# Performance work log

Hardware: AMD Instinct MI355X
Metric: run time of the kernel (lower is better)

The kernel has to match this reference:

```python
import jax, jax.numpy as jnp
import numpy as np

B, T, DIM, HEADS, MLP_H, R = 64, 197, 768, 12, 3072, 16
HD = DIM // HEADS
EPS = 1e-5
R_EFF = min(R, (T - 1) // 2)  # class token protected


def layernorm(x, g, b):
    m = jnp.mean(x, -1, keepdims=True)
    v = jnp.var(x, -1, keepdims=True)
    return (x - m) * jax.lax.rsqrt(v + EPS) * g + b


def matching_indices(metric):
    # metric: [B, T, HD]; class token (index 0 of 'a' set) protected
    metric = metric / jnp.linalg.norm(metric, axis=-1, keepdims=True)
    a, b = metric[:, ::2], metric[:, 1::2]            # [B,ta,d], [B,tb,d]
    scores = jnp.einsum('bic,bjc->bij', a, b)
    scores = scores.at[:, 0, :].set(-jnp.inf)         # protect cls token
    node_max = jnp.max(scores, axis=-1)
    node_idx = jnp.argmax(scores, axis=-1)
    edge_idx = jnp.argsort(-node_max, axis=-1)        # descending similarity
    unm_idx = edge_idx[:, R_EFF:]
    src_idx = edge_idx[:, :R_EFF]
    dst_idx = jnp.take_along_axis(node_idx, src_idx, axis=-1)
    unm_idx = jnp.sort(unm_idx, axis=1)               # keep cls first (cls token)
    return unm_idx, src_idx, dst_idx


def merge(x, unm_idx, src_idx, dst_idx):
    # x: [B, T, c] -> [B, T - R_EFF, c]; always scatter-add (as in source code)
    src, dst = x[:, ::2], x[:, 1::2]
    unm = jnp.take_along_axis(src, unm_idx[..., None], axis=1)
    sel = jnp.take_along_axis(src, src_idx[..., None], axis=1)
    bidx = jnp.arange(x.shape[0])[:, None]
    dst = dst.at[bidx, dst_idx].add(sel)
    return jnp.concatenate([unm, dst], axis=1)


def block(x, attn_size, ln1_g, ln1_b, w_qkv, w_proj, b_proj,
          ln2_g, ln2_b, w_fc1, b_fc1, w_fc2, b_fc2):
    # --- attention with log-size bias ---
    h = layernorm(x, ln1_g, ln1_b)
    qkv = (h @ w_qkv.T).reshape(B, T, 3, HEADS, HD).transpose(2, 0, 3, 1, 4)
    q, k, v = qkv[0], qkv[1], qkv[2]                  # [B,H,T,HD]
    attn = jnp.einsum('bhid,bhjd->bhij', q, k) * (HD ** -0.5)
    attn = attn + jnp.log(attn_size)[:, None, None, :, 0]
    attn = jax.nn.softmax(attn, axis=-1)
    o = jnp.einsum('bhij,bhjd->bhid', attn, v).transpose(0, 2, 1, 3).reshape(B, T, DIM)
    x = x + (o @ w_proj.T + b_proj)
    metric = jax.lax.stop_gradient(jnp.mean(k, axis=1))  # [B,T,HD]; no_grad in torch
    # --- ToMe bipartite soft matching ---
    unm_idx, src_idx, dst_idx = matching_indices(metric)
    # source tracking (adjacency initial tokens -> merged groups)
    source = jnp.broadcast_to(jnp.eye(T, dtype=x.dtype), (B, T, T))
    source = merge(source, unm_idx, src_idx, dst_idx)     # [B, Tn, T]
    tn = source.shape[1]
    rci = jnp.max(source * jnp.arange(1, tn + 1, dtype=x.dtype)[:, None], axis=-2)
    rci = (rci - 2.0)[:, 1:]                              # cls_token branch
    # size-weighted average merge
    xs = merge(x * attn_size, unm_idx, src_idx, dst_idx)
    new_size = merge(attn_size, unm_idx, src_idx, dst_idx)
    x = xs / new_size
    # --- MLP ---
    h2 = layernorm(x, ln2_g, ln2_b)
    h2 = jax.nn.gelu(h2 @ w_fc1.T + b_fc1, approximate=False)
    x = x + (h2 @ w_fc2.T + b_fc2)
    return x, new_size, rci


def setup_inputs() -> dict:
    key = jax.random.key(0)
    ks = jax.random.split(key, 6)
    return dict(
        x=jax.random.normal(ks[0], (B, T, DIM), jnp.float32),
        attn_size=jnp.ones((B, T, 1), jnp.float32),
        ln1_g=jnp.ones((DIM,), jnp.float32),
        ln1_b=jnp.zeros((DIM,), jnp.float32),
        w_qkv=jax.random.normal(ks[1], (3 * DIM, DIM), jnp.float32) * 0.02,
        w_proj=jax.random.normal(ks[2], (DIM, DIM), jnp.float32) * 0.02,
        b_proj=jnp.zeros((DIM,), jnp.float32),
        ln2_g=jnp.ones((DIM,), jnp.float32),
        ln2_b=jnp.zeros((DIM,), jnp.float32),
        w_fc1=jax.random.normal(ks[3], (MLP_H, DIM), jnp.float32) * 0.02,
        b_fc1=jnp.zeros((MLP_H,), jnp.float32),
        w_fc2=jax.random.normal(ks[4], (DIM, MLP_H), jnp.float32) * 0.02,
        b_fc2=jnp.zeros((DIM,), jnp.float32),
    )


def reference(x, attn_size, ln1_g, ln1_b, w_qkv, w_proj, b_proj,
              ln2_g, ln2_b, w_fc1, b_fc1, w_fc2, b_fc2):
    return block(x, attn_size, ln1_g, ln1_b, w_qkv, w_proj, b_proj,
                 ln2_g, ln2_b, w_fc1, b_fc1, w_fc2, b_fc2)
```

## Files before the change

kernel.cpp:

```cpp
#include <hip/hip_runtime.h>
#include <cstdint>
#include <cstddef>

#define DEVFN __device__ __forceinline__

typedef __attribute__((ext_vector_type(8))) short short8;
typedef __attribute__((ext_vector_type(4))) float f32x4;

#define GLOAD_LDS16(gaddr, laddr)                                              \
  __builtin_amdgcn_global_load_lds(                                            \
      (const __attribute__((address_space(1))) uint32_t*)(gaddr),              \
      (__attribute__((address_space(3))) uint32_t*)(laddr), 16, 0, 0)

constexpr int B_ = 64, T_ = 197, DIM_ = 768, H_ = 12, HD_ = 64, MLP_ = 3072;
constexpr int N_ = B_ * T_;
constexpr int NE_ = 99, NO_ = 98, REFF_ = 16;
constexpr int TM_ = (NE_ - REFF_) + NO_;
constexpr int NM_ = B_ * TM_;

constexpr size_t BOFF_A    = 0;
constexpr size_t BOFF_GBC  = 0;
constexpr size_t BOFF_B    = 58097664;
constexpr size_t BOFF_C    = 77463552;
constexpr size_t BOFF_D    = 113049600;
constexpr size_t BOFF_WKM  = 130842624;
constexpr size_t BOFF_RT   = 131039232;
constexpr size_t BOFF_NSZ  = 131873280;
constexpr size_t BOFF_WQB  = 131919616;
constexpr size_t BOFF_WPB  = 135458560;
constexpr size_t BOFF_W1B  = 136638208;
constexpr size_t BOFF_W2B  = 141356800;

DEVFN ushort f2b(float f) {
  union { float f; uint u; } c; c.f = f;
  uint u = c.u;
  u = (u + 0x7FFFu + ((u >> 16) & 1u)) >> 16;
  return (ushort)u;
}
DEVFN float b2f(ushort h) {
  union { uint u; float f; } c; c.u = ((uint)h) << 16;
  return c.f;
}
DEVFN uchar f2e4m3(float v) {
  return (uchar)__builtin_amdgcn_cvt_pk_fp8_f32(v, 0.f, 0, false);
}
DEVFN uint pk4_fp8(float a, float b, float c, float d) {
  int r = __builtin_amdgcn_cvt_pk_fp8_f32(a, b, 0, false);
  r = __builtin_amdgcn_cvt_pk_fp8_f32(c, d, r, true);
  return (uint)r;
}

DEVFN float fast_gelu(float x) {
  float x3 = x * x * x;
  float z2 = 2.0f * 0.7978845608028654f * fmaf(0.044715f, x3, x);
  z2 = fminf(fmaxf(z2, -60.0f), 60.0f);
  float e = __expf(z2);
  float th = (e - 1.0f) / (e + 1.0f);
  return 0.5f * x * (1.0f + th);
}

DEVFN float wave_sum(float v) {
#pragma unroll
  for (int o = 32; o; o >>= 1) v += __shfl_down(v, o, 64);
  return v;
}
DEVFN float block_sum(float v, float* red) {
  v = wave_sum(v);
  int lane = threadIdx.x & 63, wid = threadIdx.x >> 6;
  __syncthreads();
  if (lane == 0) red[wid] = v;
  __syncthreads();
  return red[0] + red[1] + red[2] + red[3];
}

constexpr int SEG0 = 3 * DIM_ * DIM_;
constexpr int SEG1 = SEG0 + DIM_ * DIM_;
constexpr int SEG2 = SEG1 + MLP_ * DIM_;
constexpr int SEG3 = SEG2 + DIM_ * MLP_;
__global__ __launch_bounds__(256) void f2ball_kernel(
    const float* __restrict__ s0, const float* __restrict__ s1,
    const float* __restrict__ s2, const float* __restrict__ s3,
    ushort* __restrict__ d0, ushort* __restrict__ d1,
    uchar* __restrict__ d2, uchar* __restrict__ d3) {
  int i = (blockIdx.x * 256 + threadIdx.x) * 4;
  if (i >= SEG3) return;
  if (i < SEG1) {
    const float* src; ushort* dst; int off;
    if (i < SEG0) { src = s0; dst = d0; off = i; }
    else          { src = s1; dst = d1; off = i - SEG0; }
    float4 v = *reinterpret_cast<const float4*>(src + off);
    ushort4 o;
    o.x = f2b(v.x); o.y = f2b(v.y); o.z = f2b(v.z); o.w = f2b(v.w);
    *reinterpret_cast<ushort4*>(dst + off) = o;
  } else {
    const float* src; uchar* dst; int off;
    if (i < SEG2) { src = s2; dst = d2; off = i - SEG1; }
    else          { src = s3; dst = d3; off = i - SEG2; }
    float4 v = *reinterpret_cast<const float4*>(src + off);
    *reinterpret_cast<uint*>(dst + off) = pk4_fp8(v.x, v.y, v.z, v.w);
  }
}

__global__ __launch_bounds__(256) void ln_kernel(
    const float* __restrict__ x, const float* __restrict__ g,
    const float* __restrict__ bb, float* __restrict__ outf,
    ushort* __restrict__ outb) {
  __shared__ float red[4];
  size_t row = blockIdx.x;
  const float* xr = x + row * DIM_;
  int tid = threadIdx.x;
  float s = 0.f;
  for (int i = tid; i < DIM_; i += 256) s += xr[i];
  s = block_sum(s, red);
  float mean = s * (1.0f / DIM_);
  float vs = 0.f;
  for (int i = tid; i < DIM_; i += 256) { float d = xr[i] - mean; vs = fmaf(d, d, vs); }
  vs = block_sum(vs, red);
  float rstd = rsqrtf(vs * (1.0f / DIM_) + 1e-5f);
  for (int i = tid; i < DIM_; i += 256) {
    float v = (xr[i] - mean) * rstd * g[i] + bb[i];
    if (outf) outf[row * DIM_ + i] = v;
    if (outb) outb[row * DIM_ + i] = f2b(v);
  }
}

__global__ __launch_bounds__(256) void wkmean_kernel(const float* __restrict__ wqkv,
                                                     float* __restrict__ wkm) {
  int idx = blockIdx.x * 256 + threadIdx.x;
  if (idx >= HD_ * DIM_) return;
  int d = idx / DIM_, c = idx % DIM_;
  float s = 0.f;
  for (int h2 = 0; h2 < H_; h2++) s += wqkv[(size_t)(DIM_ + h2 * HD_ + d) * DIM_ + c];
  wkm[idx] = s * (1.0f / H_);
}

__global__ __launch_bounds__(256) void gemm_bt(
    const float* __restrict__ A, const float* __restrict__ Bm,
    float* __restrict__ C, int M, int Nn, int K) {
  __shared__ float As[16][65];
  __shared__ float Bs[16][65];
  const int tid = threadIdx.x;
  const int tx = tid & 15, ty = tid >> 4;
  const int m0 = blockIdx.y * 64, n0 = blockIdx.x * 64;
  float acc[4][4] = {};
  for (int k0 = 0; k0 < K; k0 += 16) {
#pragma unroll
    for (int l = 0; l < 4; ++l) {
      int idx = tid + l * 256;
      int mm = idx >> 4, kk = idx & 15;
      As[kk][mm] = A[(size_t)(m0 + mm) * K + (k0 + kk)];
      Bs[kk][mm] = Bm[(size_t)(n0 + mm) * K + (k0 + kk)];
    }
    __syncthreads();
#pragma unroll
    for (int kk = 0; kk < 16; ++kk) {
      float av[4], bv[4];
#pragma unroll
      for (int i = 0; i < 4; i++) av[i] = As[kk][ty * 4 + i];
#pragma unroll
      for (int j = 0; j < 4; j++) bv[j] = Bs[kk][tx * 4 + j];
#pragma unroll
      for (int i = 0; i < 4; i++)
#pragma unroll
        for (int j = 0; j < 4; j++) acc[i][j] = fmaf(av[i], bv[j], acc[i][j]);
    }
    __syncthreads();
  }
#pragma unroll
  for (int i = 0; i < 4; i++) {
    size_t base = (size_t)(m0 + ty * 4 + i) * Nn + n0 + tx * 4;
#pragma unroll
    for (int j = 0; j < 4; j++) C[base + j] = acc[i][j];
  }
}

__global__ __launch_bounds__(256) void gemm_mfma(
    const ushort* __restrict__ A, const ushort* __restrict__ Bw,
    const float* __restrict__ bias, const float* __restrict__ res,
    float* __restrict__ Cf, ushort* __restrict__ Cb,
    int M, int Nn, int K, int act) {
  __shared__ ushort As[3][128][32];
  __shared__ ushort Bs[3][128][32];
  const int t = threadIdx.x;
  const int wid = t >> 6, l = t & 63;
  const int wrow = wid >> 1, wcol = wid & 1;
  const int lr = l & 15, lk = l >> 4;
  const int lrow = l >> 2, lseg = l & 3;
  const int sswz = lseg ^ ((lrow >> 1) & 3);
  const int rswz = (lr >> 1) & 3;

  const int nwg = (int)gridDim.x;
  const int gx = Nn >> 7;
  const int bid = (int)blockIdx.x;
  const int q = nwg >> 3, r = nwg & 7;
  const int xcd = bid & 7, sub = bid >> 3;
  const int wgid = (xcd < r ? xcd * (q + 1) : r * (q + 1) + (xcd - r) * q) + sub;
  const int m0 = (wgid / gx) * 128, n0 = (wgid % gx) * 128;

  int rA0 = m0 + wid * 32 + lrow;      rA0 = rA0 < M ? rA0 : M - 1;
  int rA1 = m0 + wid * 32 + 16 + lrow; rA1 = rA1 < M ? rA1 : M - 1;
  const ushort* gA0 = A + (size_t)rA0 * K + sswz * 8;
  const ushort* gA1 = A + (size_t)rA1 * K + sswz * 8;
  const ushort* gB0 = Bw + (size_t)(n0 + wid * 32 + lrow) * K + sswz * 8;
  const ushort* gB1 = Bw + (size_t)(n0 + wid * 32 + 16 + lrow) * K + sswz * 8;

  f32x4 acc[4][4];
#pragma unroll
  for (int i = 0; i < 4; i++)
#pragma unroll
    for (int j = 0; j < 4; j++) acc[i][j] = (f32x4){0.f, 0.f, 0.f, 0.f};

  auto STAGE = [&](int buf, int kt) {
    const int k0 = kt * 32;
    GLOAD_LDS16(gA0 + k0, &As[buf][wid * 32][0]);
    GLOAD_LDS16(gB0 + k0, &Bs[buf][wid * 32][0]);
    GLOAD_LDS16(gA1 + k0, &As[buf][wid * 32 + 16][0]);
    GLOAD_LDS16(gB1 + k0, &Bs[buf][wid * 32 + 16][0]);
  };

  const int NT = K >> 5;
  STAGE(0, 0);
  STAGE(1, 1);
  asm volatile("s_waitcnt vmcnt(4)" ::: "memory");
  __builtin_amdgcn_s_barrier();

  for (int kt = 0; kt < NT; kt++) {
    const bool ahead = (kt + 2 < NT);
    if (ahead) STAGE((kt + 2) % 3, kt + 2);
    const int cur = kt % 3;
    short8 af[4], bf[4];
#pragma unroll
    for (int mi = 0; mi < 4; mi++)
      af[mi] = *reinterpret_cast<const short8*>(
          &As[cur][wrow * 64 + mi * 16 + lr][(lk ^ rswz) * 8]);
#pragma unroll
    for (int nj = 0; nj < 4; nj++)
      bf[nj] = *reinterpret_cast<const short8*>(
          &Bs[cur][wcol * 64 + nj * 16 + lr][(lk ^ rswz) * 8]);
#pragma unroll
    for (int mi = 0; mi < 4; mi++)
#pragma unroll
      for (int nj = 0; nj < 4; nj++)
        acc[mi][nj] = __builtin_amdgcn_mfma_f32_16x16x32_bf16(af[mi], bf[nj], acc[mi][nj], 0, 0, 0);
    if (ahead) asm volatile("s_waitcnt vmcnt(4)" ::: "memory");
    else       asm volatile("s_waitcnt vmcnt(0)" ::: "memory");
    __builtin_amdgcn_s_barrier();
  }

#pragma unroll
  for (int mi = 0; mi < 4; mi++) {
    int rbase = m0 + wrow * 64 + mi * 16 + lk * 4;
#pragma unroll
    for (int nj = 0; nj < 4; nj++) {
      int col = n0 + wcol * 64 + nj * 16 + lr;
      float bv = bias ? bias[col] : 0.f;
#pragma unroll
      for (int j = 0; j < 4; j++) {
        int row = rbase + j;
        if (row >= M) continue;
        float v = acc[mi][nj][j] + bv;
        if (act) v = fast_gelu(v);
        size_t idx = (size_t)row * Nn + col;
        if (res) v += res[idx];
        if (Cf) Cf[idx] = v;
        else Cb[idx] = f2b(v);
      }
    }
  }
}

__global__ __launch_bounds__(512) void gemm_mfma_w(
    const ushort* __restrict__ A, const ushort* __restrict__ Bw,
    const float* __restrict__ bias, const float* __restrict__ res,
    float* __restrict__ Cf, ushort* __restrict__ Cb,
    int M, int Nn, int K, int act) {
  __shared__ ushort As[3][128][32];
  __shared__ ushort Bs[3][256][32];
  const int t = threadIdx.x;
  const int wid = t >> 6, l = t & 63;
  const int wm = wid >> 2, wn = wid & 3;
  const int lr = l & 15, lk = l >> 4;
  const int lrow = l >> 2, lseg = l & 3;
  const int sswz = lseg ^ ((lrow >> 1) & 3);
  const int rswz = (lr >> 1) & 3;

  const int nwg = (int)gridDim.x;
  const int gx = Nn >> 8;
  const int bid = (int)blockIdx.x;
  const int q = nwg >> 3, r = nwg & 7;
  const int xcd = bid & 7, sub = bid >> 3;
  const int wgid = (xcd < r ? xcd * (q + 1) : r * (q + 1) + (xcd - r) * q) + sub;
  const int m0 = (wgid / gx) * 128, n0 = (wgid % gx) * 256;

  int rA = m0 + wid * 16 + lrow; rA = rA < M ? rA : M - 1;
  const ushort* gA0 = A + (size_t)rA * K + sswz * 8;
  const ushort* gB0 = Bw + (size_t)(n0 + wid * 32 + lrow) * K + sswz * 8;
  const ushort* gB1 = Bw + (size_t)(n0 + wid * 32 + 16 + lrow) * K + sswz * 8;

  f32x4 acc[4][4];
#pragma unroll
  for (int i = 0; i < 4; i++)
#pragma unroll
    for (int j = 0; j < 4; j++) acc[i][j] = (f32x4){0.f, 0.f, 0.f, 0.f};

  auto STAGE = [&](int buf, int kt) {
    const int k0 = kt * 32;
    GLOAD_LDS16(gA0 + k0, &As[buf][wid * 16][0]);
    GLOAD_LDS16(gB0 + k0, &Bs[buf][wid * 32][0]);
    GLOAD_LDS16(gB1 + k0, &Bs[buf][wid * 32 + 16][0]);
  };

  const int NT = K >> 5;
  STAGE(0, 0);
  STAGE(1, 1);
  asm volatile("s_waitcnt vmcnt(3)" ::: "memory");
  __builtin_amdgcn_s_barrier();

  for (int kt = 0; kt < NT; kt++) {
    const bool ahead = (kt + 2 < NT);
    if (ahead) STAGE((kt + 2) % 3, kt + 2);
    const int cur = kt % 3;
    short8 af[4], bf[4];
#pragma unroll
    for (int mi = 0; mi < 4; mi++)
      af[mi] = *reinterpret_cast<const short8*>(
          &As[cur][wm * 64 + mi * 16 + lr][(lk ^ rswz) * 8]);
#pragma unroll
    for (int nj = 0; nj < 4; nj++)
      bf[nj] = *reinterpret_cast<const short8*>(
          &Bs[cur][wn * 64 + nj * 16 + lr][(lk ^ rswz) * 8]);
#pragma unroll
    for (int mi = 0; mi < 4; mi++)
#pragma unroll
      for (int nj = 0; nj < 4; nj++)
        acc[mi][nj] = __builtin_amdgcn_mfma_f32_16x16x32_bf16(af[mi], bf[nj], acc[mi][nj], 0, 0, 0);
    if (ahead) asm volatile("s_waitcnt vmcnt(3)" ::: "memory");
    else       asm volatile("s_waitcnt vmcnt(0)" ::: "memory");
    __builtin_amdgcn_s_barrier();
  }

#pragma unroll
  for (int mi = 0; mi < 4; mi++) {
    int rbase = m0 + wm * 64 + mi * 16 + lk * 4;
#pragma unroll
    for (int nj = 0; nj < 4; nj++) {
      int col = n0 + wn * 64 + nj * 16 + lr;
      float bv = bias ? bias[col] : 0.f;
#pragma unroll
      for (int j = 0; j < 4; j++) {
        int row = rbase + j;
        if (row >= M) continue;
        float v = acc[mi][nj][j] + bv;
        if (act) v = fast_gelu(v);
        size_t idx = (size_t)row * Nn + col;
        if (res) v += res[idx];
        if (Cf) Cf[idx] = v;
        else Cb[idx] = f2b(v);
      }
    }
  }
}

__global__ __launch_bounds__(512) void gemm_fp8_w(
    const uchar* __restrict__ A, const uchar* __restrict__ Bw,
    const float* __restrict__ bias, uchar* __restrict__ C8,
    int M, int Nn, int K) {
  __shared__ uchar As[3][128][64];
  __shared__ uchar Bs[3][256][64];
  const int t = threadIdx.x;
  const int wid = t >> 6, l = t & 63;
  const int wm = wid >> 2, wn = wid & 3;
  const int lr = l & 15, lk = l >> 4;
  const int l4 = l >> 2, lseg = l & 3;
  const int sswz = lseg ^ ((l4 >> 1) & 3);
  const int rsw2 = (lr >> 1) & 3;

  const int nwg = (int)gridDim.x;
  const int gx = Nn >> 8;
  const int bid = (int)blockIdx.x;
  const int q = nwg >> 3, r = nwg & 7;
  const int xcd = bid & 7, sub = bid >> 3;
  const int wgid = (xcd < r ? xcd * (q + 1) : r * (q + 1) + (xcd - r) * q) + sub;
  const int m0 = (wgid / gx) * 128, n0 = (wgid % gx) * 256;

  int rA = m0 + wid * 16 + l4; rA = rA < M ? rA : M - 1;
  const uchar* gA0 = A + (size_t)rA * K + sswz * 16;
  const uchar* gB0 = Bw + (size_t)(n0 + wid * 32 + l4) * K + sswz * 16;
  const uchar* gB1 = Bw + (size_t)(n0 + wid * 32 + 16 + l4) * K + sswz * 16;

  f32x4 acc[4][4];
#pragma unroll
  for (int i = 0; i < 4; i++)
#pragma unroll
    for (int j = 0; j < 4; j++) acc[i][j] = (f32x4){0.f, 0.f, 0.f, 0.f};

  auto STAGE = [&](int buf, int kt) {
    const int k0 = kt * 64;
    GLOAD_LDS16(gA0 + k0, &As[buf][wid * 16][0]);
    GLOAD_LDS16(gB0 + k0, &Bs[buf][wid * 32][0]);
    GLOAD_LDS16(gB1 + k0, &Bs[buf][wid * 32 + 16][0]);
  };

  const int NT = K >> 6;
  STAGE(0, 0);
  STAGE(1, 1);
  asm volatile("s_waitcnt vmcnt(3)" ::: "memory");
  __builtin_amdgcn_s_barrier();

  for (int kt = 0; kt < NT; kt++) {
    const bool ahead = (kt + 2 < NT);
    if (ahead) STAGE((kt + 2) % 3, kt + 2);
    const int cur = kt % 3;
#pragma unroll
    for (int ks = 0; ks < 2; ks++) {
      const int s8 = ks * 4 + lk;
      const int off = (((s8 >> 1) ^ rsw2) * 16) + (s8 & 1) * 8;
      long af[4], bf[4];
#pragma unroll
      for (int mi = 0; mi < 4; mi++)
        af[mi] = *reinterpret_cast<const long*>(&As[cur][wm * 64 + mi * 16 + lr][off]);
#pragma unroll
      for (int nj = 0; nj < 4; nj++)
        bf[nj] = *reinterpret_cast<const long*>(&Bs[cur][wn * 64 + nj * 16 + lr][off]);
#pragma unroll
      for (int mi = 0; mi < 4; mi++)
#pragma unroll
        for (int nj = 0; nj < 4; nj++)
          acc[mi][nj] = __builtin_amdgcn_mfma_f32_16x16x32_fp8_fp8(
              af[mi], bf[nj], acc[mi][nj], 0, 0, 0);
    }
    if (ahead) asm volatile("s_waitcnt vmcnt(3)" ::: "memory");
    else       asm volatile("s_waitcnt vmcnt(0)" ::: "memory");
    __builtin_amdgcn_s_barrier();
  }

#pragma unroll
  for (int mi = 0; mi < 4; mi++) {
    int rbase = m0 + wm * 64 + mi * 16 + lk * 4;
#pragma unroll
    for (int nj = 0; nj < 4; nj++) {
      int col = n0 + wn * 64 + nj * 16 + lr;
      float bv = bias[col];
#pragma unroll
      for (int j = 0; j < 4; j++) {
        int row = rbase + j;
        if (row >= M) continue;
        C8[(size_t)row * Nn + col] = f2e4m3(fast_gelu(acc[mi][nj][j] + bv));
      }
    }
  }
}

__global__ __launch_bounds__(256) void gemm_fp8(
    const uchar* __restrict__ A, const uchar* __restrict__ Bw,
    const float* __restrict__ bias, const float* __restrict__ res,
    float* __restrict__ Cf, int M, int Nn, int K) {
  __shared__ uchar As[3][128][64];
  __shared__ uchar Bs[3][128][64];
  const int t = threadIdx.x;
  const int wid = t >> 6, l = t & 63;
  const int wrow = wid >> 1, wcol = wid & 1;
  const int lr = l & 15, lk = l >> 4;
  const int l4 = l >> 2, lseg = l & 3;
  const int sswz = lseg ^ ((l4 >> 1) & 3);
  const int rsw2 = (lr >> 1) & 3;

  const int nwg = (int)gridDim.x;
  const int gx = Nn >> 7;
  const int bid = (int)blockIdx.x;
  const int q = nwg >> 3, r = nwg & 7;
  const int xcd = bid & 7, sub = bid >> 3;
  const int wgid = (xcd < r ? xcd * (q + 1) : r * (q + 1) + (xcd - r) * q) + sub;
  const int m0 = (wgid / gx) * 128, n0 = (wgid % gx) * 128;

  int rA0 = m0 + wid * 32 + l4;      rA0 = rA0 < M ? rA0 : M - 1;
  int rA1 = m0 + wid * 32 + 16 + l4; rA1 = rA1 < M ? rA1 : M - 1;
  const uchar* gA0 = A + (size_t)rA0 * K + sswz * 16;
  const uchar* gA1 = A + (size_t)rA1 * K + sswz * 16;
  const uchar* gB0 = Bw + (size_t)(n0 + wid * 32 + l4) * K + sswz * 16;
  const uchar* gB1 = Bw + (size_t)(n0 + wid * 32 + 16 + l4) * K + sswz * 16;

  f32x4 acc[4][4];
#pragma unroll
  for (int i = 0; i < 4; i++)
#pragma unroll
    for (int j = 0; j < 4; j++) acc[i][j] = (f32x4){0.f, 0.f, 0.f, 0.f};

  auto STAGE = [&](int buf, int kt) {
    const int k0 = kt * 64;
    GLOAD_LDS16(gA0 + k0, &As[buf][wid * 32][0]);
    GLOAD_LDS16(gB0 + k0, &Bs[buf][wid * 32][0]);
    GLOAD_LDS16(gA1 + k0, &As[buf][wid * 32 + 16][0]);
    GLOAD_LDS16(gB1 + k0, &Bs[buf][wid * 32 + 16][0]);
  };

  const int NT = K >> 6;
  STAGE(0, 0);
  STAGE(1, 1);
  asm volatile("s_waitcnt vmcnt(4)" ::: "memory");
  __builtin_amdgcn_s_barrier();

  for (int kt = 0; kt < NT; kt++) {
    const bool ahead = (kt + 2 < NT);
    if (ahead) STAGE((kt + 2) % 3, kt + 2);
    const int cur = kt % 3;
#pragma unroll
    for (int ks = 0; ks < 2; ks++) {
      const int s8 = ks * 4 + lk;
      const int off = (((s8 >> 1) ^ rsw2) * 16) + (s8 & 1) * 8;
      long af[4], bf[4];
#pragma unroll
      for (int mi = 0; mi < 4; mi++)
        af[mi] = *reinterpret_cast<const long*>(&As[cur][wrow * 64 + mi * 16 + lr][off]);
#pragma unroll
      for (int nj = 0; nj < 4; nj++)
        bf[nj] = *reinterpret_cast<const long*>(&Bs[cur][wcol * 64 + nj * 16 + lr][off]);
#pragma unroll
      for (int mi = 0; mi < 4; mi++)
#pragma unroll
        for (int nj = 0; nj < 4; nj++)
          acc[mi][nj] = __builtin_amdgcn_mfma_f32_16x16x32_fp8_fp8(
              af[mi], bf[nj], acc[mi][nj], 0, 0, 0);
    }
    if (ahead) asm volatile("s_waitcnt vmcnt(4)" ::: "memory");
    else       asm volatile("s_waitcnt vmcnt(0)" ::: "memory");
    __builtin_amdgcn_s_barrier();
  }

#pragma unroll
  for (int mi = 0; mi < 4; mi++) {
    int rbase = m0 + wrow * 64 + mi * 16 + lk * 4;
#pragma unroll
    for (int nj = 0; nj < 4; nj++) {
      int col = n0 + wcol * 64 + nj * 16 + lr;
      float bv = bias[col];
#pragma unroll
      for (int j = 0; j < 4; j++) {
        int row = rbase + j;
        if (row >= M) continue;
        size_t idx = (size_t)row * Nn + col;
        Cf[idx] = acc[mi][nj][j] + bv + res[idx];
      }
    }
  }
}

__global__ __launch_bounds__(512) void attn3_kernel(
    const ushort* __restrict__ qkv, const float* __restrict__ asize,
    ushort* __restrict__ o) {
  __shared__ ushort Kb[208][72];
  __shared__ ushort Vt[64][232];
  __shared__ ushort Plds[8][16][232];
  __shared__ float lb[200];
  const int bh = blockIdx.x;
  const int h = bh % H_, b = bh / H_;
  const size_t bT = (size_t)b * T_;
  const int tid = threadIdx.x;
  const int l = tid & 63, wid = tid >> 6;
  const int lr = l & 15, lk = l >> 4;

  for (int j = tid; j < T_; j += 512) lb[j] = logf(asize[bT + j]);
  for (int idx = tid; idx < 208 * 8; idx += 512) {
    int row = idx >> 3, seg = idx & 7;
    int kr = row < T_ ? row : T_ - 1;
    *reinterpret_cast<uint4*>(&Kb[row][seg * 8]) = *reinterpret_cast<const uint4*>(
        qkv + (bT + kr) * (3 * DIM_) + DIM_ + h * HD_ + seg * 8);
  }
  for (int idx = tid; idx < 197 * 8; idx += 512) {
    int row = idx >> 3, seg = idx & 7;
    uint4 v = *reinterpret_cast<const uint4*>(
        qkv + (bT + row) * (3 * DIM_) + 2 * DIM_ + h * HD_ + seg * 8);
    const ushort* us = reinterpret_cast<const ushort*>(&v);
#pragma unroll
    for (int e = 0; e < 8; e++) Vt[seg * 8 + e][row] = us[e];
  }
  for (int idx = tid; idx < 64 * 35; idx += 512) Vt[idx / 35][197 + idx % 35] = 0;
  for (int i = tid; i < 8 * 16 * 116; i += 512) reinterpret_cast<uint*>(Plds)[i] = 0;
  __syncthreads();

  for (int s = wid; s < 13; s += 8) {
    const int q0 = s * 16;
    int qr = q0 + lr; qr = qr < T_ ? qr : T_ - 1;
    const ushort* qp = qkv + (bT + qr) * (3 * DIM_) + h * HD_;
    short8 aq0 = *reinterpret_cast<const short8*>(qp + lk * 8);
    short8 aq1 = *reinterpret_cast<const short8*>(qp + 32 + lk * 8);

    f32x4 accs[13];
#pragma unroll
    for (int t2 = 0; t2 < 13; t2++) accs[t2] = (f32x4){0.f, 0.f, 0.f, 0.f};
#pragma unroll
    for (int t2 = 0; t2 < 13; t2++) {
      short8 bk0 = *reinterpret_cast<const short8*>(&Kb[t2 * 16 + lr][lk * 8]);
      short8 bk1 = *reinterpret_cast<const short8*>(&Kb[t2 * 16 + lr][32 + lk * 8]);
      accs[t2] = __builtin_amdgcn_mfma_f32_16x16x32_bf16(aq0, bk0, accs[t2], 0, 0, 0);
      accs[t2] = __builtin_amdgcn_mfma_f32_16x16x32_bf16(aq1, bk1, accs[t2], 0, 0, 0);
    }
    const int col0 = lr;
    float m4[4] = {-INFINITY, -INFINITY, -INFINITY, -INFINITY};
#pragma unroll
    for (int t2 = 0; t2 < 13; t2++) {
      int col = t2 * 16 + col0;
      bool valid = col < T_;
      float lbv = valid ? lb[col] : 0.f;
#pragma unroll
      for (int j = 0; j < 4; j++) {
        float v = valid ? fmaf(accs[t2][j], 0.125f, lbv) : -INFINITY;
        accs[t2][j] = v;
        m4[j] = fmaxf(m4[j], v);
      }
    }
#pragma unroll
    for (int off = 1; off < 16; off <<= 1)
#pragma unroll
      for (int j = 0; j < 4; j++) m4[j] = fmaxf(m4[j], __shfl_xor(m4[j], off, 64));
    float s4[4] = {0.f, 0.f, 0.f, 0.f};
#pragma unroll
    for (int t2 = 0; t2 < 13; t2++)
#pragma unroll
      for (int j = 0; j < 4; j++) {
        float e = __expf(accs[t2][j] - m4[j]);
        accs[t2][j] = e;
        s4[j] += e;
      }
#pragma unroll
    for (int off = 1; off < 16; off <<= 1)
#pragma unroll
      for (int j = 0; j < 4; j++) s4[j] += __shfl_xor(s4[j], off, 64);
    float inv4[4];
#pragma unroll
    for (int j = 0; j < 4; j++) inv4[j] = 1.0f / s4[j];
#pragma unroll
    for (int t2 = 0; t2 < 13; t2++)
#pragma unroll
      for (int j = 0; j < 4; j++)
        Plds[wid][lk * 4 + j][t2 * 16 + col0] = f2b(accs[t2][j] * inv4[j]);

    f32x4 acco[4];
#pragma unroll
    for (int ct = 0; ct < 4; ct++) acco[ct] = (f32x4){0.f, 0.f, 0.f, 0.f};
#pragma unroll
    for (int kt = 0; kt < 7; kt++) {
      short8 ap = *reinterpret_cast<const short8*>(&Plds[wid][lr][kt * 32 + lk * 8]);
#pragma unroll
      for (int ct = 0; ct < 4; ct++) {
        short8 bv = *reinterpret_cast<const short8*>(&Vt[ct * 16 + lr][kt * 32 + lk * 8]);
        acco[ct] = __builtin_amdgcn_mfma_f32_16x16x32_bf16(ap, bv, acco[ct], 0, 0, 0);
      }
    }
#pragma unroll
    for (int ct = 0; ct < 4; ct++)
#pragma unroll
      for (int j = 0; j < 4; j++) {
        int row = q0 + lk * 4 + j;
        if (row < T_)
          o[(bT + row) * DIM_ + h * HD_ + ct * 16 + lr] = f2b(acco[ct][j]);
      }
  }
}

__global__ __launch_bounds__(256) void match_kernel(
    const float* __restrict__ metric, const float* __restrict__ asize,
    int* __restrict__ route, float* __restrict__ nsz,
    float* __restrict__ out_ns, float* __restrict__ out_rci) {
  __shared__ float m[197][65];
  __shared__ float nmax[99];
  __shared__ int nidx[99];
  __shared__ int rnk[99];
  __shared__ int srcr[16];
  __shared__ int dstr[16];
  __shared__ int unmp[99];
  int b = blockIdx.x;
  int tid = threadIdx.x;
  int lane = tid & 63, wid = tid >> 6;

  if (tid < T_) {
    const float* mr = metric + ((size_t)b * T_ + tid) * HD_;
    float ss = 0.f;
#pragma unroll
    for (int d = 0; d < 64; d++) { float v = mr[d]; ss = fmaf(v, v, ss); }
    float nrm = sqrtf(ss);
#pragma unroll
    for (int d = 0; d < 64; d++) m[tid][d] = mr[d] / nrm;
  }
  __syncthreads();

  for (int i = wid; i < NE_; i += 4) {
    if (i == 0) {
      if (lane == 0) { nmax[0] = -INFINITY; nidx[0] = 0; }
      continue;
    }
    float bv = -INFINITY;
    int bj = 1 << 30;
    for (int j = lane; j < NO_; j += 64) {
      const float* a = m[2 * i];
      const float* bb = m[2 * j + 1];
      float sdot = 0.f;
#pragma unroll
      for (int d = 0; d < 64; d++) sdot = fmaf(a[d], bb[d], sdot);
      if (sdot > bv) { bv = sdot; bj = j; }
    }
#pragma unroll
    for (int off = 32; off; off >>= 1) {
      float ov = __shfl_down(bv, off, 64);
      int oj = __shfl_down(bj, off, 64);
      if (ov > bv || (ov == bv && oj < bj)) { bv = ov; bj = oj; }
    }
    if (lane == 0) { nmax[i] = bv; nidx[i] = bj; }
  }
  __syncthreads();

  if (tid < NE_) {
    float v = nmax[tid];
    int r = 0;
    for (int i2 = 0; i2 < NE_; i2++) {
      float v2 = nmax[i2];
      r += (v2 > v) || (v2 == v && i2 < tid);
    }
    rnk[tid] = r;
  }
  __syncthreads();
  if (tid < NE_ && rnk[tid] < REFF_) { srcr[rnk[tid]] = tid; dstr[rnk[tid]] = nidx[tid]; }
  __syncthreads();
  if (tid < NE_ && rnk[tid] >= REFF_) {
    int p = 0;
    for (int i2 = 0; i2 < tid; i2++) p += (rnk[i2] >= REFF_);
    unmp[tid] = p;
    int* rr = route + ((size_t)b * TM_ + p) * 18;
    rr[0] = 1;
    rr[1] = 2 * tid;
  }
  if (tid < NO_) {
    int d = tid;
    int* rr = route + ((size_t)b * TM_ + (NE_ - REFF_) + d) * 18;
    int cnt = 1;
    rr[1] = 2 * d + 1;
    for (int r = 0; r < REFF_; r++)
      if (dstr[r] == d) { cnt++; rr[cnt] = 2 * srcr[r]; }
    rr[0] = cnt;
  }
  __syncthreads();

  for (int row = tid; row < TM_; row += 256) {
    const int* rr = route + ((size_t)b * TM_ + row) * 18;
    int cnt = rr[0];
    float s = 0.f;
    for (int t2 = 0; t2 < cnt; t2++) s += asize[(size_t)b * T_ + rr[1 + t2]];
    out_ns[(size_t)b * TM_ + row] = s;
    nsz[(size_t)b * TM_ + row] = s;
  }
  for (int t = 1 + tid; t < T_; t += 256) {
    int val;
    if (t & 1) {
      val = (NE_ - REFF_ - 1) + ((t - 1) >> 1);
    } else {
      int i = t >> 1;
      val = (rnk[i] >= REFF_) ? (unmp[i] - 1) : ((NE_ - REFF_ - 1) + nidx[i]);
    }
    out_rci[(size_t)b * (T_ - 1) + (t - 1)] = (float)val;
  }
}

__global__ __launch_bounds__(256) void merge_ln_kernel(
    const float* __restrict__ x1, const float* __restrict__ asize,
    const int* __restrict__ route, const float* __restrict__ nsz,
    const float* __restrict__ g, const float* __restrict__ bb,
    float* __restrict__ xm, uchar* __restrict__ h28) {
  int row = blockIdx.x;
  int b = row / TM_;
  const int* rr = route + (size_t)row * 18;
  __shared__ int cnt_s;
  __shared__ int toks[17];
  __shared__ float szs[17];
  __shared__ float red[4];
  int tid = threadIdx.x;
  if (tid == 0) cnt_s = rr[0];
  __syncthreads();
  int cnt = cnt_s;
  if (tid < cnt) {
    int t = rr[1 + tid];
    toks[tid] = t;
    szs[tid] = asize[(size_t)b * T_ + t];
  }
  __syncthreads();
  float ns = nsz[row];
  float val[3];
#pragma unroll
  for (int p = 0; p < 3; p++) {
    int e = tid + p * 256;
    float acc = 0.f;
    for (int c2 = 0; c2 < cnt; c2++)
      acc = fmaf(x1[((size_t)b * T_ + toks[c2]) * DIM_ + e], szs[c2], acc);
    val[p] = acc / ns;
    xm[(size_t)row * DIM_ + e] = val[p];
  }
  float s = val[0] + val[1] + val[2];
  s = block_sum(s, red);
  float mean = s * (1.0f / DIM_);
  float vs = 0.f;
#pragma unroll
  for (int p = 0; p < 3; p++) { float d = val[p] - mean; vs = fmaf(d, d, vs); }
  vs = block_sum(vs, red);
  float rstd = rsqrtf(vs * (1.0f / DIM_) + 1e-5f);
#pragma unroll
  for (int p = 0; p < 3; p++) {
    int e = tid + p * 256;
    h28[(size_t)row * DIM_ + e] = f2e4m3((val[p] - mean) * rstd * g[e] + bb[e]);
  }
}

extern "C" void kernel_launch(void* const* d_in, const int* in_sizes, int n_in,
                              void* d_out, int out_size, void* d_ws, size_t ws_size,
                              hipStream_t stream) {
  const float* x_in = (const float*)d_in[0];
  const float* asize = (const float*)d_in[1];
  const float* ln1g = (const float*)d_in[2];
  const float* ln1b = (const float*)d_in[3];
  const float* wqkv = (const float*)d_in[4];
  const float* wproj = (const float*)d_in[5];
  const float* bproj = (const float*)d_in[6];
  const float* ln2g = (const float*)d_in[7];
  const float* ln2b = (const float*)d_in[8];
  const float* wfc1 = (const float*)d_in[9];
  const float* bfc1 = (const float*)d_in[10];
  const float* wfc2 = (const float*)d_in[11];
  const float* bfc2 = (const float*)d_in[12];

  char* base = (char*)d_ws;
  float* h    = (float*)(base + BOFF_A);
  ushort* qkvb = (ushort*)(base + BOFF_A);
  float* x1   = (float*)(base + BOFF_A);
  uchar* gbc8 = (uchar*)(base + BOFF_GBC);
  ushort* hb  = (ushort*)(base + BOFF_B);
  ushort* ob  = (ushort*)(base + BOFF_B);
  float* xm   = (float*)(base + BOFF_C);
  float* met  = (float*)(base + BOFF_D);
  uchar* h28  = (uchar*)(base + BOFF_D);
  float* wkm  = (float*)(base + BOFF_WKM);
  int* route  = (int*)(base + BOFF_RT);
  float* nsz  = (float*)(base + BOFF_NSZ);
  ushort* wqb = (ushort*)(base + BOFF_WQB);
  ushort* wpb = (ushort*)(base + BOFF_WPB);
  uchar* w18  = (uchar*)(base + BOFF_W1B);
  uchar* w28  = (uchar*)(base + BOFF_W2B);

  float* out_x = (float*)d_out;
  float* out_ns = out_x + (size_t)NM_ * DIM_;
  float* out_rci = out_ns + NM_;

  f2ball_kernel<<<(SEG3 / 4 + 255) / 256, 256, 0, stream>>>(
      wqkv, wproj, wfc1, wfc2, wqb, wpb, w18, w28);
  wkmean_kernel<<<(HD_ * DIM_ + 255) / 256, 256, 0, stream>>>(wqkv, wkm);

  ln_kernel<<<N_, 256, 0, stream>>>(x_in, ln1g, ln1b, h, hb);
  gemm_bt<<<dim3(1, N_ / 64), 256, 0, stream>>>(h, wkm, met, N_, HD_, DIM_);
  gemm_mfma_w<<<((N_ + 127) / 128) * (3 * DIM_ / 256), 512, 0, stream>>>(
      hb, wqb, nullptr, nullptr, nullptr, qkvb, N_, 3 * DIM_, DIM_, 0);
  attn3_kernel<<<B_ * H_, 512, 0, stream>>>(qkvb, asize, ob);
  gemm_mfma<<<(DIM_ / 128) * ((N_ + 127) / 128), 256, 0, stream>>>(
      ob, wpb, bproj, x_in, x1, nullptr, N_, DIM_, DIM_, 0);
  match_kernel<<<B_, 256, 0, stream>>>(met, asize, route, nsz, out_ns, out_rci);
  merge_ln_kernel<<<NM_, 256, 0, stream>>>(x1, asize, route, nsz, ln2g, ln2b, xm, h28);

  gemm_fp8_w<<<((NM_ + 127) / 128) * (MLP_ / 256), 512, 0, stream>>>(
      h28, w18, bfc1, gbc8, NM_, MLP_, DIM_);
  gemm_fp8<<<(DIM_ / 128) * ((NM_ + 127) / 128), 256, 0, stream>>>(
      gbc8, w28, bfc2, xm, out_x, NM_, DIM_, MLP_);
}
```

Measured before the change: 515.1 us.

## Run QKV projection in FP8 and widen FP8 GEMM LDS fragment loads

Converts the QKV weight and the first layernorm output to FP8 e4m3 and routes the QKV projection through the generalized FP8 GEMM kernel, which now optionally writes bf16 output and applies GELU only when asked. The bf16 QKV GEMM kernel is removed. Both FP8 GEMMs now load 16-byte LDS fragments once per k-tile instead of two 8-byte loads. This halves the bytes moved for the QKV GEMM and uses the faster FP8 MFMA path, at the cost of reduced precision in q/k/v that feeds attention.

```diff
diff --git a/kernel.cpp b/kernel.cpp
--- a/kernel.cpp
+++ b/kernel.cpp
@@ -6,6 +6,7 @@
 
 typedef __attribute__((ext_vector_type(8))) short short8;
 typedef __attribute__((ext_vector_type(4))) float f32x4;
+typedef __attribute__((ext_vector_type(2))) long long2v;
 
 #define GLOAD_LDS16(gaddr, laddr)                                              \
   __builtin_amdgcn_global_load_lds(                                            \
@@ -80,22 +81,21 @@
 __global__ __launch_bounds__(256) void f2ball_kernel(
     const float* __restrict__ s0, const float* __restrict__ s1,
     const float* __restrict__ s2, const float* __restrict__ s3,
-    ushort* __restrict__ d0, ushort* __restrict__ d1,
+    uchar* __restrict__ d0, ushort* __restrict__ d1,
     uchar* __restrict__ d2, uchar* __restrict__ d3) {
   int i = (blockIdx.x * 256 + threadIdx.x) * 4;
   if (i >= SEG3) return;
-  if (i < SEG1) {
-    const float* src; ushort* dst; int off;
-    if (i < SEG0) { src = s0; dst = d0; off = i; }
-    else          { src = s1; dst = d1; off = i - SEG0; }
-    float4 v = *reinterpret_cast<const float4*>(src + off);
+  if (i >= SEG0 && i < SEG1) {
+    int off = i - SEG0;
+    float4 v = *reinterpret_cast<const float4*>(s1 + off);
     ushort4 o;
     o.x = f2b(v.x); o.y = f2b(v.y); o.z = f2b(v.z); o.w = f2b(v.w);
-    *reinterpret_cast<ushort4*>(dst + off) = o;
+    *reinterpret_cast<ushort4*>(d1 + off) = o;
   } else {
     const float* src; uchar* dst; int off;
-    if (i < SEG2) { src = s2; dst = d2; off = i - SEG1; }
-    else          { src = s3; dst = d3; off = i - SEG2; }
+    if (i < SEG0)      { src = s0; dst = d0; off = i; }
+    else if (i < SEG2) { src = s2; dst = d2; off = i - SEG1; }
+    else               { src = s3; dst = d3; off = i - SEG2; }
     float4 v = *reinterpret_cast<const float4*>(src + off);
     *reinterpret_cast<uint*>(dst + off) = pk4_fp8(v.x, v.y, v.z, v.w);
   }
@@ -104,7 +104,7 @@
 __global__ __launch_bounds__(256) void ln_kernel(
     const float* __restrict__ x, const float* __restrict__ g,
     const float* __restrict__ bb, float* __restrict__ outf,
-    ushort* __restrict__ outb) {
+    uchar* __restrict__ out8) {
   __shared__ float red[4];
   size_t row = blockIdx.x;
   const float* xr = x + row * DIM_;
@@ -120,7 +120,7 @@
   for (int i = tid; i < DIM_; i += 256) {
     float v = (xr[i] - mean) * rstd * g[i] + bb[i];
     if (outf) outf[row * DIM_ + i] = v;
-    if (outb) outb[row * DIM_ + i] = f2b(v);
+    out8[row * DIM_ + i] = f2e4m3(v);
   }
 }
 
@@ -269,102 +269,10 @@
   }
 }
 
-__global__ __launch_bounds__(512) void gemm_mfma_w(
-    const ushort* __restrict__ A, const ushort* __restrict__ Bw,
-    const float* __restrict__ bias, const float* __restrict__ res,
-    float* __restrict__ Cf, ushort* __restrict__ Cb,
-    int M, int Nn, int K, int act) {
-  __shared__ ushort As[3][128][32];
-  __shared__ ushort Bs[3][256][32];
-  const int t = threadIdx.x;
-  const int wid = t >> 6, l = t & 63;
-  const int wm = wid >> 2, wn = wid & 3;
-  const int lr = l & 15, lk = l >> 4;
-  const int lrow = l >> 2, lseg = l & 3;
-  const int sswz = lseg ^ ((lrow >> 1) & 3);
-  const int rswz = (lr >> 1) & 3;
-
-  const int nwg = (int)gridDim.x;
-  const int gx = Nn >> 8;
-  const int bid = (int)blockIdx.x;
-  const int q = nwg >> 3, r = nwg & 7;
-  const int xcd = bid & 7, sub = bid >> 3;
-  const int wgid = (xcd < r ? xcd * (q + 1) : r * (q + 1) + (xcd - r) * q) + sub;
-  const int m0 = (wgid / gx) * 128, n0 = (wgid % gx) * 256;
-
-  int rA = m0 + wid * 16 + lrow; rA = rA < M ? rA : M - 1;
-  const ushort* gA0 = A + (size_t)rA * K + sswz * 8;
-  const ushort* gB0 = Bw + (size_t)(n0 + wid * 32 + lrow) * K + sswz * 8;
-  const ushort* gB1 = Bw + (size_t)(n0 + wid * 32 + 16 + lrow) * K + sswz * 8;
-
-  f32x4 acc[4][4];
-#pragma unroll
-  for (int i = 0; i < 4; i++)
-#pragma unroll
-    for (int j = 0; j < 4; j++) acc[i][j] = (f32x4){0.f, 0.f, 0.f, 0.f};
-
-  auto STAGE = [&](int buf, int kt) {
-    const int k0 = kt * 32;
-    GLOAD_LDS16(gA0 + k0, &As[buf][wid * 16][0]);
-    GLOAD_LDS16(gB0 + k0, &Bs[buf][wid * 32][0]);
-    GLOAD_LDS16(gB1 + k0, &Bs[buf][wid * 32 + 16][0]);
-  };
-
-  const int NT = K >> 5;
-  STAGE(0, 0);
-  STAGE(1, 1);
-  asm volatile("s_waitcnt vmcnt(3)" ::: "memory");
-  __builtin_amdgcn_s_barrier();
-
-  for (int kt = 0; kt < NT; kt++) {
-    const bool ahead = (kt + 2 < NT);
-    if (ahead) STAGE((kt + 2) % 3, kt + 2);
-    const int cur = kt % 3;
-    short8 af[4], bf[4];
-#pragma unroll
-    for (int mi = 0; mi < 4; mi++)
-      af[mi] = *reinterpret_cast<const short8*>(
-          &As[cur][wm * 64 + mi * 16 + lr][(lk ^ rswz) * 8]);
-#pragma unroll
-    for (int nj = 0; nj < 4; nj++)
-      bf[nj] = *reinterpret_cast<const short8*>(
-          &Bs[cur][wn * 64 + nj * 16 + lr][(lk ^ rswz) * 8]);
-#pragma unroll
-    for (int mi = 0; mi < 4; mi++)
-#pragma unroll
-      for (int nj = 0; nj < 4; nj++)
-        acc[mi][nj] = __builtin_amdgcn_mfma_f32_16x16x32_bf16(af[mi], bf[nj], acc[mi][nj], 0, 0, 0);
-    if (ahead) asm volatile("s_waitcnt vmcnt(3)" ::: "memory");
-    else       asm volatile("s_waitcnt vmcnt(0)" ::: "memory");
-    __builtin_amdgcn_s_barrier();
-  }
-
-#pragma unroll
-  for (int mi = 0; mi < 4; mi++) {
-    int rbase = m0 + wm * 64 + mi * 16 + lk * 4;
-#pragma unroll
-    for (int nj = 0; nj < 4; nj++) {
-      int col = n0 + wn * 64 + nj * 16 + lr;
-      float bv = bias ? bias[col] : 0.f;
-#pragma unroll
-      for (int j = 0; j < 4; j++) {
-        int row = rbase + j;
-        if (row >= M) continue;
-        float v = acc[mi][nj][j] + bv;
-        if (act) v = fast_gelu(v);
-        size_t idx = (size_t)row * Nn + col;
-        if (res) v += res[idx];
-        if (Cf) Cf[idx] = v;
-        else Cb[idx] = f2b(v);
-      }
-    }
-  }
-}
-
 __global__ __launch_bounds__(512) void gemm_fp8_w(
     const uchar* __restrict__ A, const uchar* __restrict__ Bw,
-    const float* __restrict__ bias, uchar* __restrict__ C8,
-    int M, int Nn, int K) {
+    const float* __restrict__ bias, ushort* __restrict__ Cb,
+    uchar* __restrict__ C8, int M, int Nn, int K, int act) {
   __shared__ uchar As[3][128][64];
   __shared__ uchar Bs[3][256][64];
   const int t = threadIdx.x;
@@ -373,7 +281,7 @@
   const int lr = l & 15, lk = l >> 4;
   const int l4 = l >> 2, lseg = l & 3;
   const int sswz = lseg ^ ((l4 >> 1) & 3);
-  const int rsw2 = (lr >> 1) & 3;
+  const int roff = (lk ^ ((lr >> 1) & 3)) * 16;
 
   const int nwg = (int)gridDim.x;
   const int gx = Nn >> 8;
@@ -411,24 +319,25 @@
     const bool ahead = (kt + 2 < NT);
     if (ahead) STAGE((kt + 2) % 3, kt + 2);
     const int cur = kt % 3;
-#pragma unroll
-    for (int ks = 0; ks < 2; ks++) {
-      const int s8 = ks * 4 + lk;
-      const int off = (((s8 >> 1) ^ rsw2) * 16) + (s8 & 1) * 8;
-      long af[4], bf[4];
-#pragma unroll
-      for (int mi = 0; mi < 4; mi++)
-        af[mi] = *reinterpret_cast<const long*>(&As[cur][wm * 64 + mi * 16 + lr][off]);
+    long2v av[4], bv[4];
+#pragma unroll
+    for (int mi = 0; mi < 4; mi++)
+      av[mi] = *reinterpret_cast<const long2v*>(&As[cur][wm * 64 + mi * 16 + lr][roff]);
+#pragma unroll
+    for (int nj = 0; nj < 4; nj++)
+      bv[nj] = *reinterpret_cast<const long2v*>(&Bs[cur][wn * 64 + nj * 16 + lr][roff]);
+#pragma unroll
+    for (int mi = 0; mi < 4; mi++)
 #pragma unroll
       for (int nj = 0; nj < 4; nj++)
-        bf[nj] = *reinterpret_cast<const long*>(&Bs[cur][wn * 64 + nj * 16 + lr][off]);
-#pragma unroll
-      for (int mi = 0; mi < 4; mi++)
-#pragma unroll
-        for (int nj = 0; nj < 4; nj++)
-          acc[mi][nj] = __builtin_amdgcn_mfma_f32_16x16x32_fp8_fp8(
-              af[mi], bf[nj], acc[mi][nj], 0, 0, 0);
-    }
+        acc[mi][nj] = __builtin_amdgcn_mfma_f32_16x16x32_fp8_fp8(
+            av[mi].x, bv[nj].x, acc[mi][nj], 0, 0, 0);
+#pragma unroll
+    for (int mi = 0; mi < 4; mi++)
+#pragma unroll
+      for (int nj = 0; nj < 4; nj++)
+        acc[mi][nj] = __builtin_amdgcn_mfma_f32_16x16x32_fp8_fp8(
+            av[mi].y, bv[nj].y, acc[mi][nj], 0, 0, 0);
     if (ahead) asm volatile("s_waitcnt vmcnt(3)" ::: "memory");
     else       asm volatile("s_waitcnt vmcnt(0)" ::: "memory");
     __builtin_amdgcn_s_barrier();
@@ -440,12 +349,16 @@
 #pragma unroll
     for (int nj = 0; nj < 4; nj++) {
       int col = n0 + wn * 64 + nj * 16 + lr;
-      float bv = bias[col];
+      float bvv = bias ? bias[col] : 0.f;
 #pragma unroll
       for (int j = 0; j < 4; j++) {
         int row = rbase + j;
         if (row >= M) continue;
-        C8[(size_t)row * Nn + col] = f2e4m3(fast_gelu(acc[mi][nj][j] + bv));
+        float v = acc[mi][nj][j] + bvv;
+        if (act) v = fast_gelu(v);
+        size_t idx = (size_t)row * Nn + col;
+        if (Cb) Cb[idx] = f2b(v);
+        else C8[idx] = f2e4m3(v);
       }
     }
   }
@@ -463,7 +376,7 @@
   const int lr = l & 15, lk = l >> 4;
   const int l4 = l >> 2, lseg = l & 3;
   const int sswz = lseg ^ ((l4 >> 1) & 3);
-  const int rsw2 = (lr >> 1) & 3;
+  const int roff = (lk ^ ((lr >> 1) & 3)) * 16;
 
   const int nwg = (int)gridDim.x;
   const int gx = Nn >> 7;
@@ -504,24 +417,25 @@
     const bool ahead = (kt + 2 < NT);
     if (ahead) STAGE((kt + 2) % 3, kt + 2);
     const int cur = kt % 3;
-#pragma unroll
-    for (int ks = 0; ks < 2; ks++) {
-      const int s8 = ks * 4 + lk;
-      const int off = (((s8 >> 1) ^ rsw2) * 16) + (s8 & 1) * 8;
-      long af[4], bf[4];
-#pragma unroll
-      for (int mi = 0; mi < 4; mi++)
-        af[mi] = *reinterpret_cast<const long*>(&As[cur][wrow * 64 + mi * 16 + lr][off]);
+    long2v av[4], bv[4];
+#pragma unroll
+    for (int mi = 0; mi < 4; mi++)
+      av[mi] = *reinterpret_cast<const long2v*>(&As[cur][wrow * 64 + mi * 16 + lr][roff]);
+#pragma unroll
+    for (int nj = 0; nj < 4; nj++)
+      bv[nj] = *reinterpret_cast<const long2v*>(&Bs[cur][wcol * 64 + nj * 16 + lr][roff]);
+#pragma unroll
+    for (int mi = 0; mi < 4; mi++)
 #pragma unroll
       for (int nj = 0; nj < 4; nj++)
-        bf[nj] = *reinterpret_cast<const long*>(&Bs[cur][wcol * 64 + nj * 16 + lr][off]);
-#pragma unroll
-      for (int mi = 0; mi < 4; mi++)
-#pragma unroll
-        for (int nj = 0; nj < 4; nj++)
-          acc[mi][nj] = __builtin_amdgcn_mfma_f32_16x16x32_fp8_fp8(
-              af[mi], bf[nj], acc[mi][nj], 0, 0, 0);
-    }
+        acc[mi][nj] = __builtin_amdgcn_mfma_f32_16x16x32_fp8_fp8(
+            av[mi].x, bv[nj].x, acc[mi][nj], 0, 0, 0);
+#pragma unroll
+    for (int mi = 0; mi < 4; mi++)
+#pragma unroll
+      for (int nj = 0; nj < 4; nj++)
+        acc[mi][nj] = __builtin_amdgcn_mfma_f32_16x16x32_fp8_fp8(
+            av[mi].y, bv[nj].y, acc[mi][nj], 0, 0, 0);
     if (ahead) asm volatile("s_waitcnt vmcnt(4)" ::: "memory");
     else       asm volatile("s_waitcnt vmcnt(0)" ::: "memory");
     __builtin_amdgcn_s_barrier();
@@ -533,13 +447,13 @@
 #pragma unroll
     for (int nj = 0; nj < 4; nj++) {
       int col = n0 + wcol * 64 + nj * 16 + lr;
-      float bv = bias[col];
+      float bvv = bias[col];
 #pragma unroll
       for (int j = 0; j < 4; j++) {
         int row = rbase + j;
         if (row >= M) continue;
         size_t idx = (size_t)row * Nn + col;
-        Cf[idx] = acc[mi][nj][j] + bv + res[idx];
+        Cf[idx] = acc[mi][nj][j] + bvv + res[idx];
       }
     }
   }
@@ -830,7 +744,7 @@
   ushort* qkvb = (ushort*)(base + BOFF_A);
   float* x1   = (float*)(base + BOFF_A);
   uchar* gbc8 = (uchar*)(base + BOFF_GBC);
-  ushort* hb  = (ushort*)(base + BOFF_B);
+  uchar* h8   = (uchar*)(base + BOFF_B);
   ushort* ob  = (ushort*)(base + BOFF_B);
   float* xm   = (float*)(base + BOFF_C);
   float* met  = (float*)(base + BOFF_D);
@@ -838,7 +752,7 @@
   float* wkm  = (float*)(base + BOFF_WKM);
   int* route  = (int*)(base + BOFF_RT);
   float* nsz  = (float*)(base + BOFF_NSZ);
-  ushort* wqb = (ushort*)(base + BOFF_WQB);
+  uchar* w8q  = (uchar*)(base + BOFF_WQB);
   ushort* wpb = (ushort*)(base + BOFF_WPB);
   uchar* w18  = (uchar*)(base + BOFF_W1B);
   uchar* w28  = (uchar*)(base + BOFF_W2B);
@@ -848,13 +762,13 @@
   float* out_rci = out_ns + NM_;
 
   f2ball_kernel<<<(SEG3 / 4 + 255) / 256, 256, 0, stream>>>(
-      wqkv, wproj, wfc1, wfc2, wqb, wpb, w18, w28);
+      wqkv, wproj, wfc1, wfc2, w8q, wpb, w18, w28);
   wkmean_kernel<<<(HD_ * DIM_ + 255) / 256, 256, 0, stream>>>(wqkv, wkm);
 
-  ln_kernel<<<N_, 256, 0, stream>>>(x_in, ln1g, ln1b, h, hb);
+  ln_kernel<<<N_, 256, 0, stream>>>(x_in, ln1g, ln1b, h, h8);
   gemm_bt<<<dim3(1, N_ / 64), 256, 0, stream>>>(h, wkm, met, N_, HD_, DIM_);
-  gemm_mfma_w<<<((N_ + 127) / 128) * (3 * DIM_ / 256), 512, 0, stream>>>(
-      hb, wqb, nullptr, nullptr, nullptr, qkvb, N_, 3 * DIM_, DIM_, 0);
+  gemm_fp8_w<<<((N_ + 127) / 128) * (3 * DIM_ / 256), 512, 0, stream>>>(
+      h8, w8q, nullptr, qkvb, nullptr, N_, 3 * DIM_, DIM_, 0);
   attn3_kernel<<<B_ * H_, 512, 0, stream>>>(qkvb, asize, ob);
   gemm_mfma<<<(DIM_ / 128) * ((N_ + 127) / 128), 256, 0, stream>>>(
       ob, wpb, bproj, x_in, x1, nullptr, N_, DIM_, DIM_, 0);
@@ -862,7 +776,7 @@
   merge_ln_kernel<<<NM_, 256, 0, stream>>>(x1, asize, route, nsz, ln2g, ln2b, xm, h28);
 
   gemm_fp8_w<<<((NM_ + 127) / 128) * (MLP_ / 256), 512, 0, stream>>>(
-      h28, w18, bfc1, gbc8, NM_, MLP_, DIM_);
+      h28, w18, bfc1, nullptr, gbc8, NM_, MLP_, DIM_, 1);
   gemm_fp8<<<(DIM_ / 128) * ((NM_ + 127) / 128), 256, 0, stream>>>(
       gbc8, w28, bfc2, xm, out_x, NM_, DIM_, MLP_);
 }
```

After: 502.6 us. -2.4%, faster.
